# Performance work log

Measured on AMD Instinct MI355X. Metric: run time of the kernel, lower is better.

The kernel has to match this reference:

```python
import jax, jax.numpy as jnp
import numpy as np

D = 256      # input_size == output_size
H = 8        # head_count
DH = D // H  # dim per head


def setup_inputs() -> dict:
    key = jax.random.key(0)
    ks = jax.random.split(key, 11)
    s = 1.0 / np.sqrt(D)
    inp = {
        "x": jax.random.normal(ks[0], (4, 2048, D), dtype=jnp.float32),
        "Wq": jax.random.normal(ks[1], (D, D), dtype=jnp.float32) * s,
        "bq": jnp.zeros((D,), jnp.float32),
        "Wk": jax.random.normal(ks[2], (D, D), dtype=jnp.float32) * s,
        "bk": jnp.zeros((D,), jnp.float32),
        "Wv": jax.random.normal(ks[3], (D, D), dtype=jnp.float32) * s,
        "bv": jnp.zeros((D,), jnp.float32),
        "Wo": jax.random.normal(ks[4], (D, D), dtype=jnp.float32) * s,
        "bo": jnp.zeros((D,), jnp.float32),
        "Wc": jax.random.normal(ks[5], (D, D), dtype=jnp.float32) * s,
        "bc": jnp.zeros((D,), jnp.float32),
    }
    return inp


def _split_heads(t):
    b, n, _ = t.shape
    return t.reshape(b, n, H, DH).transpose(0, 2, 1, 3)  # b h n dh


def reference(x, Wq, bq, Wk, bk, Wv, bv, Wo, bo, Wc, bc):
    # Multi-head self-attention over all nodes (complete graph)
    q = _split_heads(x @ Wq + bq)
    k = _split_heads(x @ Wk + bk)
    v = _split_heads(x @ Wv + bv)
    scale = 1.0 / jnp.sqrt(jnp.asarray(DH, x.dtype))
    scores = jnp.einsum("bhqd,bhkd->bhqk", q * scale, k)
    attn = jax.nn.softmax(scores, axis=-1)  # attn dropout = identity (eval)
    ctx = jnp.einsum("bhqk,bhkd->bhqd", attn, v)
    b, _, n, _ = ctx.shape
    ctx = ctx.transpose(0, 2, 1, 3).reshape(b, n, D)
    ctx = ctx @ Wo + bo  # MHA output projection
    # linear_context + dropout (identity in eval) + residual
    out = x + (ctx @ Wc + bc)
    return out
```

## Files before the change

### kernel.cpp

```cpp
#include <hip/hip_runtime.h>

#define DMODEL 256
#define HEADS 8
#define DHEAD 32
#define NSEQ 2048
#define BATCH 4
#define MTOT (BATCH*NSEQ)

typedef __bf16 bf16x8 __attribute__((ext_vector_type(8)));
typedef float f32x4 __attribute__((ext_vector_type(4)));

#define CS 0.25507282111989365f

__device__ __forceinline__ unsigned short f2bf(float f) {
    union { float f; unsigned int u; } v; v.f = f;
    unsigned int u = v.u;
    unsigned int r = u + 0x7FFFu + ((u >> 16) & 1u);
    return (unsigned short)(r >> 16);
}

__device__ __forceinline__ unsigned pkbf(float a, float b) {
    union { __bf16 h[2]; unsigned u; } t;
    t.h[0] = (__bf16)a; t.h[1] = (__bf16)b;
    return t.u;
}

__device__ __forceinline__ f32x4 mfma16(bf16x8 a, bf16x8 b, f32x4 c) {
    return __builtin_amdgcn_mfma_f32_16x16x32_bf16(a, b, c, 0, 0, 0);
}

#define GLD16(g, l) __builtin_amdgcn_global_load_lds( \
    (const __attribute__((address_space(1))) unsigned int*)(g), \
    (__attribute__((address_space(3))) unsigned int*)(l), 16, 0, 0)

__global__ __launch_bounds__(256) void prep_kernel(
    const float* __restrict__ x,
    const float* __restrict__ Wq, const float* __restrict__ Wk,
    const float* __restrict__ Wv, const float* __restrict__ Wo,
    const float* __restrict__ Wc,
    const float* __restrict__ bq, const float* __restrict__ bk,
    const float* __restrict__ bv, const float* __restrict__ bo,
    const float* __restrict__ bc,
    unsigned short* __restrict__ xbf,
    unsigned short* __restrict__ Wt,
    float* __restrict__ bcat,
    unsigned short* __restrict__ Woct,
    float* __restrict__ bocf)
{
    const int tid = threadIdx.x;
    if (blockIdx.x < 257) {
        int k = blockIdx.x;
        int n = tid;
        const float* arow = (k < 256) ? (Wo + k * 256) : bo;
        float a0 = 0.f, a1 = 0.f, a2 = 0.f, a3 = 0.f;
#pragma unroll 4
        for (int j = 0; j < 256; j += 4) {
            a0 = fmaf(arow[j],     Wc[j * 256 + n],       a0);
            a1 = fmaf(arow[j + 1], Wc[(j + 1) * 256 + n], a1);
            a2 = fmaf(arow[j + 2], Wc[(j + 2) * 256 + n], a2);
            a3 = fmaf(arow[j + 3], Wc[(j + 3) * 256 + n], a3);
        }
        float acc = (a0 + a1) + (a2 + a3);
        if (k < 256) Woct[n * 256 + k] = f2bf(acc);
        else         bocf[n] = acc + bc[n];
        return;
    }
    if (blockIdx.x < 2305) {
        int idx = (blockIdx.x - 257) * 256 + tid;
        float4 v = reinterpret_cast<const float4*>(x)[idx];
        ushort4 o;
        o.x = f2bf(v.x); o.y = f2bf(v.y); o.z = f2bf(v.z); o.w = f2bf(v.w);
        reinterpret_cast<ushort4*>(xbf)[idx] = o;
        return;
    }
    if (blockIdx.x < 2385) {
        __shared__ unsigned short Lt[64 * 72];
        const int bb = blockIdx.x - 2305;
        const int wid = tid >> 6, lane = tid & 63;
        const int n0 = (bb >> 2) * 64, k0 = (bb & 3) * 64;
        const float* Wsrc; int col0;
        if (n0 < 256)       { Wsrc = Wq; col0 = n0; }
        else if (n0 < 512)  { Wsrc = Wk; col0 = n0 - 256; }
        else if (n0 < 768)  { Wsrc = Wv; col0 = n0 - 512; }
        else if (n0 < 1024) { Wsrc = Wo; col0 = n0 - 768; }
        else                { Wsrc = Wc; col0 = n0 - 1024; }
#pragma unroll
        for (int r = 0; r < 16; ++r) {
            int k = k0 + wid * 16 + r;
            Lt[lane * 72 + wid * 16 + r] = f2bf(Wsrc[k * 256 + col0 + lane]);
        }
        __syncthreads();
#pragma unroll
        for (int c = tid; c < 512; c += 256) {
            int row = c >> 3, seg = c & 7;
            *reinterpret_cast<bf16x8*>(Wt + (n0 + row) * 256 + k0 + seg * 8) =
                *reinterpret_cast<const bf16x8*>(Lt + row * 72 + seg * 8);
        }
        return;
    }
    int t = (blockIdx.x - 2385) * 256 + tid;
    if (t < 1280) {
        float v;
        if (t < 256)       v = bq[t];
        else if (t < 512)  v = bk[t - 256];
        else if (t < 768)  v = bv[t - 512];
        else if (t < 1024) v = bo[t - 768];
        else               v = bc[t - 1024];
        bcat[t] = v;
    }
}

__global__ __launch_bounds__(256) void gemm_qkv(
    const unsigned short* __restrict__ A,
    const unsigned short* __restrict__ Wt,
    const float* __restrict__ bias,
    unsigned short* __restrict__ outQ,
    unsigned short* __restrict__ outK,
    unsigned short* __restrict__ outVt)
{
    __shared__ __align__(16) unsigned short Bl[64 * 256];
    const int tid = threadIdx.x;
    const int wid = tid >> 6;
    const int lane = tid & 63;
    const int lo = lane & 15, hi = lane >> 4;
    const int m0 = blockIdx.x * 128 + wid * 32;
    const int n0 = blockIdx.y * 64;

#pragma unroll
    for (int j = 0; j < 8; ++j) {
        int chunkbase = (j * 4 + wid) * 64;
        int chunk = chunkbase + lane;
        int row = chunk >> 5, Jp = chunk & 31;
        int J = (Jp & 24) | ((Jp ^ row) & 7);
        GLD16(Wt + (n0 + row) * 256 + J * 8, Bl + chunkbase * 8);
    }
    asm volatile("s_waitcnt vmcnt(0)" ::: "memory");
    __syncthreads();

    const unsigned short* arow0 = A + (m0 + lo) * 256 + hi * 8;
    f32x4 acc[2][4] = {};
#pragma unroll
    for (int s = 0; s < 8; ++s) {
        bf16x8 a0 = *reinterpret_cast<const bf16x8*>(arow0 + s * 32);
        bf16x8 a1 = *reinterpret_cast<const bf16x8*>(arow0 + 16 * 256 + s * 32);
        int Jp = ((s >> 1) << 3) | ((((s & 1) << 2) + hi) ^ (lo & 7));
#pragma unroll
        for (int n = 0; n < 4; ++n) {
            bf16x8 b = *reinterpret_cast<const bf16x8*>(
                Bl + (n * 16 + lo) * 256 + Jp * 8);
            acc[0][n] = mfma16(a0, b, acc[0][n]);
            acc[1][n] = mfma16(a1, b, acc[1][n]);
        }
    }

    const int type = blockIdx.y >> 2;
    const int m0b = blockIdx.x * 128;
    unsigned short* Lb = Bl;
    __syncthreads();
    if (type < 2) {
#pragma unroll
        for (int mf = 0; mf < 2; ++mf)
#pragma unroll
        for (int n = 0; n < 4; ++n) {
            float bs = bias[n0 + n * 16 + lo];
#pragma unroll
            for (int i = 0; i < 4; ++i) {
                float val = acc[mf][n][i] + bs;
                if (type == 0) val *= CS;
                Lb[(wid * 32 + mf * 16 + hi * 4 + i) * 72 + n * 16 + lo] = f2bf(val);
            }
        }
    } else {
#pragma unroll
        for (int mf = 0; mf < 2; ++mf)
#pragma unroll
        for (int n = 0; n < 4; ++n) {
            float bs = bias[n0 + n * 16 + lo];
            uint2 pk;
            pk.x = pkbf(acc[mf][n][0] + bs, acc[mf][n][1] + bs);
            pk.y = pkbf(acc[mf][n][2] + bs, acc[mf][n][3] + bs);
            *reinterpret_cast<uint2*>(
                Lb + (n * 16 + lo) * 136 + wid * 32 + mf * 16 + hi * 4) = pk;
        }
    }
    __syncthreads();
    if (type < 2) {
        unsigned short* outP = (type == 0) ? outQ : outK;
#pragma unroll
        for (int r = 0; r < 4; ++r) {
            int cid = r * 256 + tid;
            int m_l = cid >> 3, seg = cid & 7;
            bf16x8 chunk = *reinterpret_cast<const bf16x8*>(Lb + m_l * 72 + seg * 8);
            int m = m0b + m_l, gc = n0 + seg * 8;
            int b = m >> 11, nn = m & 2047, hh = (gc >> 5) & 7, dh = gc & 31;
            *reinterpret_cast<bf16x8*>(
                outP + (((b * 8) + hh) * 2048 + nn) * 32 + dh) = chunk;
        }
    } else {
#pragma unroll
        for (int r = 0; r < 4; ++r) {
            int cid = r * 256 + tid;
            int gcl = cid >> 4, seg = cid & 15;
            bf16x8 chunk = *reinterpret_cast<const bf16x8*>(Lb + gcl * 136 + seg * 8);
            int gc = n0 + gcl, m = m0b + seg * 8;
            int b = m >> 11, nn = m & 2047, hh = (gc >> 5) & 7, dh = gc & 31;
            *reinterpret_cast<bf16x8*>(
                outVt + (((b * 8) + hh) * 32 + dh) * 2048 + nn) = chunk;
        }
    }
}

__global__ __launch_bounds__(256, 4) void attn_kernel(
    const unsigned short* __restrict__ Q,
    const unsigned short* __restrict__ K,
    const unsigned short* __restrict__ Vt,
    unsigned short* __restrict__ ctx)
{
    __shared__ __align__(16) char smem[32768];

    const int tid = threadIdx.x;
    const int wid = tid >> 6;
    const int lane = tid & 63;
    const int lo = lane & 15, hi = lane >> 4;

    const int bid = blockIdx.x;
    const int bh = ((bid >> 7) << 3) | (bid & 7);
    const int qt = (bid >> 3) & 15;
    const int q0 = qt * 128 + wid * 32;

    const unsigned short* Qb = Q + bh * (NSEQ * 32);
    const unsigned short* Kb = K + bh * (NSEQ * 32);
    const unsigned short* Vb = Vt + bh * (32 * NSEQ);

    bf16x8 qfA = *reinterpret_cast<const bf16x8*>(Qb + (q0 + lo) * 32 + hi * 8);
    bf16x8 qfB = *reinterpret_cast<const bf16x8*>(Qb + (q0 + 16 + lo) * 32 + hi * 8);

    const int lt = tid;
    const unsigned short* ksrc0 = Kb + (2 * (lt >> 3) + ((lt >> 2) & 1)) * 32
                                     + ((lt & 3) ^ ((lt >> 3) & 3)) * 8;
    const unsigned short* ksrc1 = ksrc0 + 64 * 32;
    const unsigned short* vsrc0 = Vb + (lt >> 3) * NSEQ
                                     + ((lt & 7) ^ ((lt >> 3) & 7)) * 8;
    const unsigned short* vsrc1 = vsrc0 + 64;
    char* kdst = smem + lt * 16;
    char* vdst = smem + 16384 + lt * 16;

    f32x4 o0A = {}, o1A = {}, odA = {};
    f32x4 o0B = {}, o1B = {}, odB = {};
    const f32x4 z = {};
    const int prs = lo & 7;
    const int kxor = (hi ^ ((lo >> 1) & 3)) * 8;

    union { unsigned u[4]; bf16x8 v; } ones;
    ones.u[0] = 0x3F803F80u; ones.u[1] = 0x3F803F80u;
    ones.u[2] = 0x3F803F80u; ones.u[3] = 0x3F803F80u;

#define STAGE_T(tt, buf) do { \
    GLD16(ksrc0 + (tt) * 4096, kdst + (buf) * 8192); \
    GLD16(ksrc1 + (tt) * 4096, kdst + (buf) * 8192 + 4096); \
    GLD16(vsrc0 + (tt) * 128,  vdst + (buf) * 8192); \
    GLD16(vsrc1 + (tt) * 128,  vdst + (buf) * 8192 + 4096); \
} while (0)

    STAGE_T(0, 0);
    asm volatile("s_waitcnt vmcnt(0)" ::: "memory");
    __builtin_amdgcn_s_barrier();
    __builtin_amdgcn_sched_barrier(0);

    int cur = 0;
    for (int t = 0; t < 16; ++t) {
        if (t < 15) STAGE_T(t + 1, cur ^ 1);
        const unsigned short* Kc = (const unsigned short*)(smem + cur * 8192);
        const unsigned short* Vc = (const unsigned short*)(smem + 16384 + cur * 8192);

        __builtin_amdgcn_s_setprio(1);
#pragma unroll
        for (int h2 = 0; h2 < 2; ++h2) {
            const unsigned short* Kh = Kc + h2 * 2048;
            const unsigned short* Vh = Vc + h2 * 2048;
            f32x4 sA[4], sB[4];
#pragma unroll
            for (int c = 0; c < 4; ++c) {
                bf16x8 kf = *reinterpret_cast<const bf16x8*>(
                    Kh + (c * 16 + lo) * 32 + kxor);
                sA[c] = mfma16(kf, qfA, z);
                sB[c] = mfma16(kf, qfB, z);
            }
#pragma unroll
            for (int kk = 0; kk < 2; ++kk) {
                unsigned uA = pkbf(__builtin_amdgcn_exp2f(sA[2 * kk][0]),
                                   __builtin_amdgcn_exp2f(sA[2 * kk][1]));
                unsigned uB = pkbf(__builtin_amdgcn_exp2f(sA[2 * kk][2]),
                                   __builtin_amdgcn_exp2f(sA[2 * kk][3]));
                unsigned uC = pkbf(__builtin_amdgcn_exp2f(sA[2 * kk + 1][0]),
                                   __builtin_amdgcn_exp2f(sA[2 * kk + 1][1]));
                unsigned uD = pkbf(__builtin_amdgcn_exp2f(sA[2 * kk + 1][2]),
                                   __builtin_amdgcn_exp2f(sA[2 * kk + 1][3]));
                auto r1 = __builtin_amdgcn_permlane32_swap(uA, uC, false, false);
                auto r2 = __builtin_amdgcn_permlane16_swap(r1[0], r1[1], false, false);
                auto r3 = __builtin_amdgcn_permlane32_swap(uB, uD, false, false);
                auto r4 = __builtin_amdgcn_permlane16_swap(r3[0], r3[1], false, false);
                union { unsigned u[4]; bf16x8 v; } pbA;
                pbA.u[0] = r2[0]; pbA.u[1] = r4[0]; pbA.u[2] = r2[1]; pbA.u[3] = r4[1];

                unsigned wA = pkbf(__builtin_amdgcn_exp2f(sB[2 * kk][0]),
                                   __builtin_amdgcn_exp2f(sB[2 * kk][1]));
                unsigned wB = pkbf(__builtin_amdgcn_exp2f(sB[2 * kk][2]),
                                   __builtin_amdgcn_exp2f(sB[2 * kk][3]));
                unsigned wC = pkbf(__builtin_amdgcn_exp2f(sB[2 * kk + 1][0]),
                                   __builtin_amdgcn_exp2f(sB[2 * kk + 1][1]));
                unsigned wD = pkbf(__builtin_amdgcn_exp2f(sB[2 * kk + 1][2]),
                                   __builtin_amdgcn_exp2f(sB[2 * kk + 1][3]));
                auto t1 = __builtin_amdgcn_permlane32_swap(wA, wC, false, false);
                auto t2 = __builtin_amdgcn_permlane16_swap(t1[0], t1[1], false, false);
                auto t3 = __builtin_amdgcn_permlane32_swap(wB, wD, false, false);
                auto t4 = __builtin_amdgcn_permlane16_swap(t3[0], t3[1], false, false);
                union { unsigned u[4]; bf16x8 v; } pbB;
                pbB.u[0] = t2[0]; pbB.u[1] = t4[0]; pbB.u[2] = t2[1]; pbB.u[3] = t4[1];

                int sw = ((4 * kk + hi) ^ prs) * 8;
                bf16x8 a0 = *reinterpret_cast<const bf16x8*>(Vh + lo * 64 + sw);
                bf16x8 a1 = *reinterpret_cast<const bf16x8*>(Vh + (16 + lo) * 64 + sw);
                o0A = mfma16(a0, pbA.v, o0A);
                o1A = mfma16(a1, pbA.v, o1A);
                odA = mfma16(ones.v, pbA.v, odA);
                o0B = mfma16(a0, pbB.v, o0B);
                o1B = mfma16(a1, pbB.v, o1B);
                odB = mfma16(ones.v, pbB.v, odB);
            }
        }
        __builtin_amdgcn_s_setprio(0);

        if (t < 15) {
            asm volatile("s_waitcnt vmcnt(0)" ::: "memory");
            __builtin_amdgcn_s_barrier();
            __builtin_amdgcn_sched_barrier(0);
            cur ^= 1;
        }
    }

    float invA = 1.0f / odA[0];
    float invB = 1.0f / odB[0];
    const int b = bh >> 3, h = bh & 7;
    unsigned short* dstA = ctx + (size_t)((b * 2048 + q0 + lo)) * 256 + h * 32;
    unsigned short* dstB = dstA + 16 * 256;
    ushort4 w0, w1;
    w0.x = f2bf(o0A[0] * invA); w0.y = f2bf(o0A[1] * invA);
    w0.z = f2bf(o0A[2] * invA); w0.w = f2bf(o0A[3] * invA);
    w1.x = f2bf(o1A[0] * invA); w1.y = f2bf(o1A[1] * invA);
    w1.z = f2bf(o1A[2] * invA); w1.w = f2bf(o1A[3] * invA);
    *reinterpret_cast<ushort4*>(dstA + hi * 4)      = w0;
    *reinterpret_cast<ushort4*>(dstA + 16 + hi * 4) = w1;
    w0.x = f2bf(o0B[0] * invB); w0.y = f2bf(o0B[1] * invB);
    w0.z = f2bf(o0B[2] * invB); w0.w = f2bf(o0B[3] * invB);
    w1.x = f2bf(o1B[0] * invB); w1.y = f2bf(o1B[1] * invB);
    w1.z = f2bf(o1B[2] * invB); w1.w = f2bf(o1B[3] * invB);
    *reinterpret_cast<ushort4*>(dstB + hi * 4)      = w0;
    *reinterpret_cast<ushort4*>(dstB + 16 + hi * 4) = w1;
#undef STAGE_T
}

__global__ __launch_bounds__(256) void gemm_ctx(
    const unsigned short* __restrict__ A,
    const unsigned short* __restrict__ Wt,
    const float* __restrict__ boc,
    const float* __restrict__ xres,
    float* __restrict__ outF)
{
    __shared__ __align__(16) unsigned short Bl[64 * 256];
    const int tid = threadIdx.x;
    const int wid = tid >> 6;
    const int lane = tid & 63;
    const int lo = lane & 15, hi = lane >> 4;
    const int m0 = blockIdx.x * 128 + wid * 32;
    const int n0 = blockIdx.y * 64;

#pragma unroll
    for (int j = 0; j < 8; ++j) {
        int chunkbase = (j * 4 + wid) * 64;
        int chunk = chunkbase + lane;
        int row = chunk >> 5, Jp = chunk & 31;
        int J = (Jp & 24) | ((Jp ^ row) & 7);
        GLD16(Wt + (n0 + row) * 256 + J * 8, Bl + chunkbase * 8);
    }
    asm volatile("s_waitcnt vmcnt(0)" ::: "memory");
    __syncthreads();

    const unsigned short* arow0 = A + (m0 + lo) * 256 + hi * 8;
    f32x4 acc[2][4] = {};
#pragma unroll
    for (int s = 0; s < 8; ++s) {
        bf16x8 a0 = *reinterpret_cast<const bf16x8*>(arow0 + s * 32);
        bf16x8 a1 = *reinterpret_cast<const bf16x8*>(arow0 + 16 * 256 + s * 32);
        int Jp = ((s >> 1) << 3) | ((((s & 1) << 2) + hi) ^ (lo & 7));
#pragma unroll
        for (int n = 0; n < 4; ++n) {
            bf16x8 b = *reinterpret_cast<const bf16x8*>(
                Bl + (n * 16 + lo) * 256 + Jp * 8);
            acc[0][n] = mfma16(a0, b, acc[0][n]);
            acc[1][n] = mfma16(a1, b, acc[1][n]);
        }
    }
#pragma unroll
    for (int mf = 0; mf < 2; ++mf) {
        const int row_base = m0 + mf * 16 + hi * 4;
#pragma unroll
        for (int n = 0; n < 4; ++n) {
            int gc = n0 + n * 16 + lo;
            float bs = boc[gc];
#pragma unroll
            for (int i = 0; i < 4; ++i)
                outF[(row_base + i) * 256 + gc] =
                    xres[(row_base + i) * 256 + gc] + acc[mf][n][i] + bs;
        }
    }
}

extern "C" void kernel_launch(void* const* d_in, const int* in_sizes, int n_in,
                              void* d_out, int out_size, void* d_ws, size_t ws_size,
                              hipStream_t stream) {
    const float* x  = (const float*)d_in[0];
    const float* Wq = (const float*)d_in[1];
    const float* bq = (const float*)d_in[2];
    const float* Wk = (const float*)d_in[3];
    const float* bk = (const float*)d_in[4];
    const float* Wv = (const float*)d_in[5];
    const float* bv = (const float*)d_in[6];
    const float* Wo = (const float*)d_in[7];
    const float* bo = (const float*)d_in[8];
    const float* Wc = (const float*)d_in[9];
    const float* bc = (const float*)d_in[10];
    float* out = (float*)d_out;

    char* p = (char*)d_ws;
    unsigned short* xbf  = (unsigned short*)p;  p += (size_t)MTOT * DMODEL * 2;
    unsigned short* Wt   = (unsigned short*)p;  p += (size_t)1280 * 256 * 2;
    float* bcat          = (float*)p;           p += (size_t)1280 * 4;
    unsigned short* Qw   = (unsigned short*)p;  p += (size_t)32 * 2048 * 32 * 2;
    unsigned short* Kw   = (unsigned short*)p;  p += (size_t)32 * 2048 * 32 * 2;
    unsigned short* Vtw  = (unsigned short*)p;  p += (size_t)32 * 32 * 2048 * 2;
    unsigned short* ctx  = (unsigned short*)p;  p += (size_t)MTOT * DMODEL * 2;
    unsigned short* Woct = (unsigned short*)p;  p += (size_t)256 * 256 * 2;
    float* bocf          = (float*)p;           p += (size_t)256 * 4;

    prep_kernel<<<2390, 256, 0, stream>>>(x, Wq, Wk, Wv, Wo, Wc,
                                          bq, bk, bv, bo, bc,
                                          xbf, Wt, bcat, Woct, bocf);
    gemm_qkv<<<dim3(64, 12), 256, 0, stream>>>(xbf, Wt, bcat, Qw, Kw, Vtw);
    attn_kernel<<<512, 256, 0, stream>>>(Qw, Kw, Vtw, ctx);
    gemm_ctx<<<dim3(64, 4), 256, 0, stream>>>(ctx, Woct, bocf, x, out);
}
```

Measured before the change: 62.99 us.

## Load K/V fragments directly from global into registers, drop LDS staging

```diff
diff --git a/kernel.cpp b/kernel.cpp
--- a/kernel.cpp
+++ b/kernel.cpp
@@ -210,14 +210,12 @@
     }
 }
 
-__global__ __launch_bounds__(256, 4) void attn_kernel(
+__global__ __launch_bounds__(256, 3) void attn_kernel(
     const unsigned short* __restrict__ Q,
     const unsigned short* __restrict__ K,
     const unsigned short* __restrict__ Vt,
     unsigned short* __restrict__ ctx)
 {
-    __shared__ __align__(16) char smem[32768];
-
     const int tid = threadIdx.x;
     const int wid = tid >> 6;
     const int lane = tid & 63;
@@ -229,114 +227,92 @@
     const int q0 = qt * 128 + wid * 32;
 
     const unsigned short* Qb = Q + bh * (NSEQ * 32);
-    const unsigned short* Kb = K + bh * (NSEQ * 32);
-    const unsigned short* Vb = Vt + bh * (32 * NSEQ);
+    const unsigned short* kp = K + bh * (NSEQ * 32) + lo * 32 + hi * 8;
+    const unsigned short* vp = Vt + bh * (32 * NSEQ) + lo * NSEQ + hi * 8;
 
     bf16x8 qfA = *reinterpret_cast<const bf16x8*>(Qb + (q0 + lo) * 32 + hi * 8);
     bf16x8 qfB = *reinterpret_cast<const bf16x8*>(Qb + (q0 + 16 + lo) * 32 + hi * 8);
-
-    const int lt = tid;
-    const unsigned short* ksrc0 = Kb + (2 * (lt >> 3) + ((lt >> 2) & 1)) * 32
-                                     + ((lt & 3) ^ ((lt >> 3) & 3)) * 8;
-    const unsigned short* ksrc1 = ksrc0 + 64 * 32;
-    const unsigned short* vsrc0 = Vb + (lt >> 3) * NSEQ
-                                     + ((lt & 7) ^ ((lt >> 3) & 7)) * 8;
-    const unsigned short* vsrc1 = vsrc0 + 64;
-    char* kdst = smem + lt * 16;
-    char* vdst = smem + 16384 + lt * 16;
 
     f32x4 o0A = {}, o1A = {}, odA = {};
     f32x4 o0B = {}, o1B = {}, odB = {};
     const f32x4 z = {};
-    const int prs = lo & 7;
-    const int kxor = (hi ^ ((lo >> 1) & 3)) * 8;
 
     union { unsigned u[4]; bf16x8 v; } ones;
     ones.u[0] = 0x3F803F80u; ones.u[1] = 0x3F803F80u;
     ones.u[2] = 0x3F803F80u; ones.u[3] = 0x3F803F80u;
 
-#define STAGE_T(tt, buf) do { \
-    GLD16(ksrc0 + (tt) * 4096, kdst + (buf) * 8192); \
-    GLD16(ksrc1 + (tt) * 4096, kdst + (buf) * 8192 + 4096); \
-    GLD16(vsrc0 + (tt) * 128,  vdst + (buf) * 8192); \
-    GLD16(vsrc1 + (tt) * 128,  vdst + (buf) * 8192 + 4096); \
+#define LOADK(R0, R1, R2, R3, base) do { \
+    R0 = *reinterpret_cast<const bf16x8*>((base));        \
+    R1 = *reinterpret_cast<const bf16x8*>((base) + 512);  \
+    R2 = *reinterpret_cast<const bf16x8*>((base) + 1024); \
+    R3 = *reinterpret_cast<const bf16x8*>((base) + 1536); \
 } while (0)
 
-    STAGE_T(0, 0);
-    asm volatile("s_waitcnt vmcnt(0)" ::: "memory");
-    __builtin_amdgcn_s_barrier();
-    __builtin_amdgcn_sched_barrier(0);
-
-    int cur = 0;
-    for (int t = 0; t < 16; ++t) {
-        if (t < 15) STAGE_T(t + 1, cur ^ 1);
-        const unsigned short* Kc = (const unsigned short*)(smem + cur * 8192);
-        const unsigned short* Vc = (const unsigned short*)(smem + 16384 + cur * 8192);
-
+#define LOADV(base) do { \
+    v0 = *reinterpret_cast<const bf16x8*>((base));                  \
+    v1 = *reinterpret_cast<const bf16x8*>((base) + 16 * NSEQ);      \
+    v2 = *reinterpret_cast<const bf16x8*>((base) + 32);             \
+    v3 = *reinterpret_cast<const bf16x8*>((base) + 16 * NSEQ + 32); \
+} while (0)
+
+#define PVKK(S0, S1, T0, T1, A0, A1) do { \
+    unsigned uA = pkbf(__builtin_amdgcn_exp2f(S0[0]), __builtin_amdgcn_exp2f(S0[1])); \
+    unsigned uB = pkbf(__builtin_amdgcn_exp2f(S0[2]), __builtin_amdgcn_exp2f(S0[3])); \
+    unsigned uC = pkbf(__builtin_amdgcn_exp2f(S1[0]), __builtin_amdgcn_exp2f(S1[1])); \
+    unsigned uD = pkbf(__builtin_amdgcn_exp2f(S1[2]), __builtin_amdgcn_exp2f(S1[3])); \
+    auto r1 = __builtin_amdgcn_permlane32_swap(uA, uC, false, false); \
+    auto r2 = __builtin_amdgcn_permlane16_swap(r1[0], r1[1], false, false); \
+    auto r3 = __builtin_amdgcn_permlane32_swap(uB, uD, false, false); \
+    auto r4 = __builtin_amdgcn_permlane16_swap(r3[0], r3[1], false, false); \
+    union { unsigned u[4]; bf16x8 v; } pbA; \
+    pbA.u[0] = r2[0]; pbA.u[1] = r4[0]; pbA.u[2] = r2[1]; pbA.u[3] = r4[1]; \
+    unsigned wA = pkbf(__builtin_amdgcn_exp2f(T0[0]), __builtin_amdgcn_exp2f(T0[1])); \
+    unsigned wB = pkbf(__builtin_amdgcn_exp2f(T0[2]), __builtin_amdgcn_exp2f(T0[3])); \
+    unsigned wC = pkbf(__builtin_amdgcn_exp2f(T1[0]), __builtin_amdgcn_exp2f(T1[1])); \
+    unsigned wD = pkbf(__builtin_amdgcn_exp2f(T1[2]), __builtin_amdgcn_exp2f(T1[3])); \
+    auto t1 = __builtin_amdgcn_permlane32_swap(wA, wC, false, false); \
+    auto t2 = __builtin_amdgcn_permlane16_swap(t1[0], t1[1], false, false); \
+    auto t3 = __builtin_amdgcn_permlane32_swap(wB, wD, false, false); \
+    auto t4 = __builtin_amdgcn_permlane16_swap(t3[0], t3[1], false, false); \
+    union { unsigned u[4]; bf16x8 v; } pbB; \
+    pbB.u[0] = t2[0]; pbB.u[1] = t4[0]; pbB.u[2] = t2[1]; pbB.u[3] = t4[1]; \
+    o0A = mfma16(A0, pbA.v, o0A); \
+    o1A = mfma16(A1, pbA.v, o1A); \
+    odA = mfma16(ones.v, pbA.v, odA); \
+    o0B = mfma16(A0, pbB.v, o0B); \
+    o1B = mfma16(A1, pbB.v, o1B); \
+    odB = mfma16(ones.v, pbB.v, odB); \
+} while (0)
+
+#define TILE(K0, K1, K2, K3) do { \
+    f32x4 sA0 = mfma16(K0, qfA, z); f32x4 sB0 = mfma16(K0, qfB, z); \
+    f32x4 sA1 = mfma16(K1, qfA, z); f32x4 sB1 = mfma16(K1, qfB, z); \
+    f32x4 sA2 = mfma16(K2, qfA, z); f32x4 sB2 = mfma16(K2, qfB, z); \
+    f32x4 sA3 = mfma16(K3, qfA, z); f32x4 sB3 = mfma16(K3, qfB, z); \
+    PVKK(sA0, sA1, sB0, sB1, v0, v1); \
+    PVKK(sA2, sA3, sB2, sB3, v2, v3); \
+} while (0)
+
+    bf16x8 kx0, kx1, kx2, kx3;
+    bf16x8 ky0, ky1, ky2, ky3;
+    bf16x8 v0, v1, v2, v3;
+
+    LOADK(kx0, kx1, kx2, kx3, kp);
+
+    for (int it = 0; it < 16; ++it) {
+        LOADV(vp);
+        LOADK(ky0, ky1, ky2, ky3, kp + 2048);
         __builtin_amdgcn_s_setprio(1);
-#pragma unroll
-        for (int h2 = 0; h2 < 2; ++h2) {
-            const unsigned short* Kh = Kc + h2 * 2048;
-            const unsigned short* Vh = Vc + h2 * 2048;
-            f32x4 sA[4], sB[4];
-#pragma unroll
-            for (int c = 0; c < 4; ++c) {
-                bf16x8 kf = *reinterpret_cast<const bf16x8*>(
-                    Kh + (c * 16 + lo) * 32 + kxor);
-                sA[c] = mfma16(kf, qfA, z);
-                sB[c] = mfma16(kf, qfB, z);
-            }
-#pragma unroll
-            for (int kk = 0; kk < 2; ++kk) {
-                unsigned uA = pkbf(__builtin_amdgcn_exp2f(sA[2 * kk][0]),
-                                   __builtin_amdgcn_exp2f(sA[2 * kk][1]));
-                unsigned uB = pkbf(__builtin_amdgcn_exp2f(sA[2 * kk][2]),
-                                   __builtin_amdgcn_exp2f(sA[2 * kk][3]));
-                unsigned uC = pkbf(__builtin_amdgcn_exp2f(sA[2 * kk + 1][0]),
-                                   __builtin_amdgcn_exp2f(sA[2 * kk + 1][1]));
-                unsigned uD = pkbf(__builtin_amdgcn_exp2f(sA[2 * kk + 1][2]),
-                                   __builtin_amdgcn_exp2f(sA[2 * kk + 1][3]));
-                auto r1 = __builtin_amdgcn_permlane32_swap(uA, uC, false, false);
-                auto r2 = __builtin_amdgcn_permlane16_swap(r1[0], r1[1], false, false);
-                auto r3 = __builtin_amdgcn_permlane32_swap(uB, uD, false, false);
-                auto r4 = __builtin_amdgcn_permlane16_swap(r3[0], r3[1], false, false);
-                union { unsigned u[4]; bf16x8 v; } pbA;
-                pbA.u[0] = r2[0]; pbA.u[1] = r4[0]; pbA.u[2] = r2[1]; pbA.u[3] = r4[1];
-
-                unsigned wA = pkbf(__builtin_amdgcn_exp2f(sB[2 * kk][0]),
-                                   __builtin_amdgcn_exp2f(sB[2 * kk][1]));
-                unsigned wB = pkbf(__builtin_amdgcn_exp2f(sB[2 * kk][2]),
-                                   __builtin_amdgcn_exp2f(sB[2 * kk][3]));
-                unsigned wC = pkbf(__builtin_amdgcn_exp2f(sB[2 * kk + 1][0]),
-                                   __builtin_amdgcn_exp2f(sB[2 * kk + 1][1]));
-                unsigned wD = pkbf(__builtin_amdgcn_exp2f(sB[2 * kk + 1][2]),
-                                   __builtin_amdgcn_exp2f(sB[2 * kk + 1][3]));
-                auto t1 = __builtin_amdgcn_permlane32_swap(wA, wC, false, false);
-                auto t2 = __builtin_amdgcn_permlane16_swap(t1[0], t1[1], false, false);
-                auto t3 = __builtin_amdgcn_permlane32_swap(wB, wD, false, false);
-                auto t4 = __builtin_amdgcn_permlane16_swap(t3[0], t3[1], false, false);
-                union { unsigned u[4]; bf16x8 v; } pbB;
-                pbB.u[0] = t2[0]; pbB.u[1] = t4[0]; pbB.u[2] = t2[1]; pbB.u[3] = t4[1];
-
-                int sw = ((4 * kk + hi) ^ prs) * 8;
-                bf16x8 a0 = *reinterpret_cast<const bf16x8*>(Vh + lo * 64 + sw);
-                bf16x8 a1 = *reinterpret_cast<const bf16x8*>(Vh + (16 + lo) * 64 + sw);
-                o0A = mfma16(a0, pbA.v, o0A);
-                o1A = mfma16(a1, pbA.v, o1A);
-                odA = mfma16(ones.v, pbA.v, odA);
-                o0B = mfma16(a0, pbB.v, o0B);
-                o1B = mfma16(a1, pbB.v, o1B);
-                odB = mfma16(ones.v, pbB.v, odB);
-            }
-        }
+        TILE(kx0, kx1, kx2, kx3);
         __builtin_amdgcn_s_setprio(0);
-
-        if (t < 15) {
-            asm volatile("s_waitcnt vmcnt(0)" ::: "memory");
-            __builtin_amdgcn_s_barrier();
-            __builtin_amdgcn_sched_barrier(0);
-            cur ^= 1;
-        }
+        vp += 64;
+        LOADV(vp);
+        if (it < 15) LOADK(kx0, kx1, kx2, kx3, kp + 4096);
+        __builtin_amdgcn_s_setprio(1);
+        TILE(ky0, ky1, ky2, ky3);
+        __builtin_amdgcn_s_setprio(0);
+        vp += 64;
+        kp += 4096;
     }
 
     float invA = 1.0f / odA[0];
@@ -357,7 +333,10 @@
     w1.z = f2bf(o1B[2] * invB); w1.w = f2bf(o1B[3] * invB);
     *reinterpret_cast<ushort4*>(dstB + hi * 4)      = w0;
     *reinterpret_cast<ushort4*>(dstB + 16 + hi * 4) = w1;
-#undef STAGE_T
+#undef LOADK
+#undef LOADV
+#undef PVKK
+#undef TILE
 }
 
 __global__ __launch_bounds__(256) void gemm_ctx(
```

After: 77.34 us. 22.8% more time.

## Pre-permute V^T key order in projection to drop permlane swaps in attention

Applied to the files above, without the earlier changes.

```diff
diff --git a/kernel.cpp b/kernel.cpp
--- a/kernel.cpp
+++ b/kernel.cpp
@@ -201,11 +201,15 @@
         for (int r = 0; r < 4; ++r) {
             int cid = r * 256 + tid;
             int gcl = cid >> 4, seg = cid & 15;
-            bf16x8 chunk = *reinterpret_cast<const bf16x8*>(Lb + gcl * 136 + seg * 8);
+            const unsigned short* src = Lb + gcl * 136 + seg * 8;
+            uint2 lo4 = *reinterpret_cast<const uint2*>(src);
+            uint2 hi4 = *reinterpret_cast<const uint2*>(src + 4);
             int gc = n0 + gcl, m = m0b + seg * 8;
             int b = m >> 11, nn = m & 2047, hh = (gc >> 5) & 7, dh = gc & 31;
-            *reinterpret_cast<bf16x8*>(
-                outVt + (((b * 8) + hh) * 32 + dh) * 2048 + nn) = chunk;
+            int pos0 = (nn & ~63) | (nn & 32) | ((nn & 8) << 1) | ((nn & 16) >> 2);
+            unsigned short* dst = outVt + (((b * 8) + hh) * 32 + dh) * 2048;
+            *reinterpret_cast<uint2*>(dst + pos0)     = lo4;
+            *reinterpret_cast<uint2*>(dst + pos0 + 8) = hi4;
         }
     }
 }
@@ -262,6 +266,25 @@
     GLD16(vsrc1 + (tt) * 128,  vdst + (buf) * 8192 + 4096); \
 } while (0)
 
+#define PVKK(S0, S1, T0, T1, A0, A1) do { \
+    union { unsigned u[4]; bf16x8 v; } pbA; \
+    pbA.u[0] = pkbf(__builtin_amdgcn_exp2f(S0[0]), __builtin_amdgcn_exp2f(S0[1])); \
+    pbA.u[1] = pkbf(__builtin_amdgcn_exp2f(S0[2]), __builtin_amdgcn_exp2f(S0[3])); \
+    pbA.u[2] = pkbf(__builtin_amdgcn_exp2f(S1[0]), __builtin_amdgcn_exp2f(S1[1])); \
+    pbA.u[3] = pkbf(__builtin_amdgcn_exp2f(S1[2]), __builtin_amdgcn_exp2f(S1[3])); \
+    union { unsigned u[4]; bf16x8 v; } pbB; \
+    pbB.u[0] = pkbf(__builtin_amdgcn_exp2f(T0[0]), __builtin_amdgcn_exp2f(T0[1])); \
+    pbB.u[1] = pkbf(__builtin_amdgcn_exp2f(T0[2]), __builtin_amdgcn_exp2f(T0[3])); \
+    pbB.u[2] = pkbf(__builtin_amdgcn_exp2f(T1[0]), __builtin_amdgcn_exp2f(T1[1])); \
+    pbB.u[3] = pkbf(__builtin_amdgcn_exp2f(T1[2]), __builtin_amdgcn_exp2f(T1[3])); \
+    o0A = mfma16(A0, pbA.v, o0A); \
+    o1A = mfma16(A1, pbA.v, o1A); \
+    odA = mfma16(ones.v, pbA.v, odA); \
+    o0B = mfma16(A0, pbB.v, o0B); \
+    o1B = mfma16(A1, pbB.v, o1B); \
+    odB = mfma16(ones.v, pbB.v, odB); \
+} while (0)
+
     STAGE_T(0, 0);
     asm volatile("s_waitcnt vmcnt(0)" ::: "memory");
     __builtin_amdgcn_s_barrier();
@@ -288,45 +311,10 @@
             }
 #pragma unroll
             for (int kk = 0; kk < 2; ++kk) {
-                unsigned uA = pkbf(__builtin_amdgcn_exp2f(sA[2 * kk][0]),
-                                   __builtin_amdgcn_exp2f(sA[2 * kk][1]));
-                unsigned uB = pkbf(__builtin_amdgcn_exp2f(sA[2 * kk][2]),
-                                   __builtin_amdgcn_exp2f(sA[2 * kk][3]));
-                unsigned uC = pkbf(__builtin_amdgcn_exp2f(sA[2 * kk + 1][0]),
-                                   __builtin_amdgcn_exp2f(sA[2 * kk + 1][1]));
-                unsigned uD = pkbf(__builtin_amdgcn_exp2f(sA[2 * kk + 1][2]),
-                                   __builtin_amdgcn_exp2f(sA[2 * kk + 1][3]));
-                auto r1 = __builtin_amdgcn_permlane32_swap(uA, uC, false, false);
-                auto r2 = __builtin_amdgcn_permlane16_swap(r1[0], r1[1], false, false);
-                auto r3 = __builtin_amdgcn_permlane32_swap(uB, uD, false, false);
-                auto r4 = __builtin_amdgcn_permlane16_swap(r3[0], r3[1], false, false);
-                union { unsigned u[4]; bf16x8 v; } pbA;
-                pbA.u[0] = r2[0]; pbA.u[1] = r4[0]; pbA.u[2] = r2[1]; pbA.u[3] = r4[1];
-
-                unsigned wA = pkbf(__builtin_amdgcn_exp2f(sB[2 * kk][0]),
-                                   __builtin_amdgcn_exp2f(sB[2 * kk][1]));
-                unsigned wB = pkbf(__builtin_amdgcn_exp2f(sB[2 * kk][2]),
-                                   __builtin_amdgcn_exp2f(sB[2 * kk][3]));
-                unsigned wC = pkbf(__builtin_amdgcn_exp2f(sB[2 * kk + 1][0]),
-                                   __builtin_amdgcn_exp2f(sB[2 * kk + 1][1]));
-                unsigned wD = pkbf(__builtin_amdgcn_exp2f(sB[2 * kk + 1][2]),
-                                   __builtin_amdgcn_exp2f(sB[2 * kk + 1][3]));
-                auto t1 = __builtin_amdgcn_permlane32_swap(wA, wC, false, false);
-                auto t2 = __builtin_amdgcn_permlane16_swap(t1[0], t1[1], false, false);
-                auto t3 = __builtin_amdgcn_permlane32_swap(wB, wD, false, false);
-                auto t4 = __builtin_amdgcn_permlane16_swap(t3[0], t3[1], false, false);
-                union { unsigned u[4]; bf16x8 v; } pbB;
-                pbB.u[0] = t2[0]; pbB.u[1] = t4[0]; pbB.u[2] = t2[1]; pbB.u[3] = t4[1];
-
                 int sw = ((4 * kk + hi) ^ prs) * 8;
                 bf16x8 a0 = *reinterpret_cast<const bf16x8*>(Vh + lo * 64 + sw);
                 bf16x8 a1 = *reinterpret_cast<const bf16x8*>(Vh + (16 + lo) * 64 + sw);
-                o0A = mfma16(a0, pbA.v, o0A);
-                o1A = mfma16(a1, pbA.v, o1A);
-                odA = mfma16(ones.v, pbA.v, odA);
-                o0B = mfma16(a0, pbB.v, o0B);
-                o1B = mfma16(a1, pbB.v, o1B);
-                odB = mfma16(ones.v, pbB.v, odB);
+                PVKK(sA[2 * kk], sA[2 * kk + 1], sB[2 * kk], sB[2 * kk + 1], a0, a1);
             }
         }
         __builtin_amdgcn_s_setprio(0);
@@ -358,6 +346,7 @@
     *reinterpret_cast<ushort4*>(dstB + hi * 4)      = w0;
     *reinterpret_cast<ushort4*>(dstB + 16 + hi * 4) = w1;
 #undef STAGE_T
+#undef PVKK
 }
 
 __global__ __launch_bounds__(256) void gemm_ctx(
```

Result: faster. 59.49 us (-5.6%).
